# Kernel tuning notes

Hardware: AMD Instinct MI355X
Metric: run time of the kernel (lower is better)

Reference implementation:

```python
import jax, jax.numpy as jnp
import numpy as np

C_IN, C_OUT, K = 64, 64, 3
KK = K * K


def _conv3x3(x, w, b):
    # x: [B, Cin, H, W], w: [Cout, Cin, 3, 3], b: [Cout] or None. stride 1, pad 1.
    y = jax.lax.conv_general_dilated(
        x, w, window_strides=(1, 1), padding=((1, 1), (1, 1)),
        dimension_numbers=("NCHW", "OIHW", "NCHW"))
    if b is not None:
        y = y + b[None, :, None, None]
    return y


def _deform_conv2d(x, offset, mask, weight):
    # torchvision.ops.deform_conv2d with stride=1, pad=1, dilation=1, 1 offset group.
    # x: [B,C,H,W]; offset: [B,2*KK,H,W] (per-tap (dy,dx)); mask: [B,KK,H,W];
    # weight: [O,C,K,K]
    B, C, H, W = x.shape
    O = weight.shape[0]
    ky, kx = jnp.meshgrid(jnp.arange(K), jnp.arange(K), indexing="ij")
    hs = jnp.arange(H)
    ws = jnp.arange(W)
    # base sample positions per tap k=(ky*K+kx): [KK,H,W]
    base_y = (hs[:, None] - 1)[None] + ky.reshape(KK, 1, 1)
    base_x = (ws[None, :] - 1)[None] + kx.reshape(KK, 1, 1)
    off = offset.reshape(B, KK, 2, H, W)
    py = base_y[None].astype(x.dtype) + off[:, :, 0]  # [B,KK,H,W]
    px = base_x[None].astype(x.dtype) + off[:, :, 1]

    y0 = jnp.floor(py)
    x0 = jnp.floor(px)
    wy = py - y0  # bilinear fractional weights
    wx = px - x0
    y0i = y0.astype(jnp.int32)
    x0i = x0.astype(jnp.int32)

    imflat = x.reshape(B, C, H * W)

    def gather_b(im, idx):  # im: [C,HW], idx: [KK,H,W] -> [C,KK,H,W]
        return im[:, idx]

    val = jnp.zeros((B, C, KK, H, W), x.dtype)
    for dy, dx in ((0, 0), (0, 1), (1, 0), (1, 1)):
        yc = y0i + dy
        xc = x0i + dx
        valid = ((yc >= 0) & (yc < H) & (xc >= 0) & (xc < W)).astype(x.dtype)
        cw = (wy if dy else (1.0 - wy)) * (wx if dx else (1.0 - wx)) * valid
        idx = jnp.clip(yc, 0, H - 1) * W + jnp.clip(xc, 0, W - 1)
        g = jax.vmap(gather_b)(imflat, idx)  # [B,C,KK,H,W]
        val = val + cw[:, None] * g
    val = val * mask[:, None]  # modulation
    # contract 9-tap patches with conv weight
    return jnp.einsum("bckhw,ock->bohw", val, weight.reshape(O, C, KK))


def setup_inputs() -> dict:
    key = jax.random.key(0)
    ks = jax.random.split(key, 8)
    B, H, W = 4, 96, 96
    cin2 = 2 * C_IN + 2
    frame_i = jax.random.normal(ks[0], (B, C_IN, H, W), jnp.float32)
    frame_j = jax.random.normal(ks[1], (B, C_IN, H, W), jnp.float32)
    flow_ij = jax.random.normal(ks[2], (B, 2, H, W), jnp.float32)
    # small random weights so offsets are nonzero (zero-init would degenerate)
    w_off = jax.random.normal(ks[3], (2 * KK, cin2, K, K), jnp.float32) * 0.01
    b_off = jax.random.normal(ks[4], (2 * KK,), jnp.float32) * 0.1
    w_mod = jax.random.normal(ks[5], (KK, cin2, K, K), jnp.float32) * 0.01
    b_mod = jax.random.normal(ks[6], (KK,), jnp.float32) * 0.1
    w_reg = jax.random.normal(ks[7], (C_OUT, C_IN, K, K), jnp.float32) * (1.0 / np.sqrt(C_IN * KK))
    return {"frame_i": frame_i, "frame_j": frame_j, "flow_ij": flow_ij,
            "w_off": w_off, "b_off": b_off, "w_mod": w_mod, "b_mod": b_mod,
            "w_reg": w_reg}


def reference(frame_i, frame_j, flow_ij, w_off, b_off, w_mod, b_mod, w_reg):
    offset_input = jnp.concatenate([frame_i, frame_j, flow_ij], axis=1)
    offset = _conv3x3(offset_input, w_off, b_off)            # [B,2*KK,H,W]
    modulator = 2.0 * jax.nn.sigmoid(_conv3x3(offset_input, w_mod, b_mod))  # [B,KK,H,W]
    return _deform_conv2d(frame_j, offset, modulator, w_reg)
```

## Files before the change

### kernel.cpp

```cpp
#include <hip/hip_runtime.h>
#include <math.h>

#define BB   4
#define HH   96
#define WW   96
#define HW   (HH * WW)
#define CIN  64
#define COUT 64
#define C2B  192
#define NROW (BB * HW)
#define ZROW NROW
#define NSTRIP (NROW / 16)
#define BPX3 (NSTRIP / 8)
#define NA   (9 * 5 * 2 * 512)
#define NW   (9 * 2 * 4 * 512)
#define PXB2 (NROW / 32)
#define PWBLK 324
#define TSX  35
#define PR   55

typedef short v8s __attribute__((ext_vector_type(8)));
typedef float v4f __attribute__((ext_vector_type(4)));

__device__ __forceinline__ unsigned short f2bf(float f) {
    unsigned u = __float_as_uint(f);
    return (unsigned short)((u + 0x7FFFu + ((u >> 16) & 1u)) >> 16);
}
__device__ __forceinline__ unsigned pack2(float a, float b) {
    return (unsigned)f2bf(a) | ((unsigned)f2bf(b) << 16);
}
__device__ __forceinline__ unsigned bil2(unsigned a, unsigned b, unsigned c,
                                         unsigned d, float w00, float w01,
                                         float w10, float w11) {
    float lo = w00 * __uint_as_float(a << 16) + w01 * __uint_as_float(b << 16)
             + w10 * __uint_as_float(c << 16) + w11 * __uint_as_float(d << 16);
    float hi = w00 * __uint_as_float(a & 0xffff0000u)
             + w01 * __uint_as_float(b & 0xffff0000u)
             + w10 * __uint_as_float(c & 0xffff0000u)
             + w11 * __uint_as_float(d & 0xffff0000u);
    return pack2(lo, hi);
}

__global__ __launch_bounds__(256) void prep_kernel(
    const float* __restrict__ fi, const float* __restrict__ fj,
    const float* __restrict__ fl, const float* __restrict__ w_off,
    const float* __restrict__ w_mod, const float* __restrict__ w_reg,
    unsigned short* __restrict__ xt, unsigned short* __restrict__ wa2f,
    unsigned short* __restrict__ wb2f)
{
    int blk = blockIdx.x;
    if (blk < PXB2) {
        __shared__ __align__(16) unsigned tile[64 * TSX];
        int tid = threadIdx.x;
        int p = tid & 63, cg = tid >> 6;
        int u = blk >> 1, half = blk & 1;
        int r0 = u * 64;
        int b = r0 / HW;
        int hw = r0 - b * HW + p;
        uint4* dst = (uint4*)(xt + (size_t)r0 * C2B);
        if (half == 0) {
            const float* pi = fi + (size_t)b * CIN * HW + hw;
#pragma unroll
            for (int d = 0; d < 8; ++d) {
                int c = cg * 16 + 2 * d;
                tile[p * TSX + cg * 8 + d] =
                    pack2(pi[(size_t)c * HW], pi[(size_t)(c + 1) * HW]);
            }
            __syncthreads();
#pragma unroll
            for (int i = 0; i < 2; ++i) {
                int gq = i * 256 + tid;
                int rl = gq >> 3, c4 = gq & 7;
                const unsigned* s = &tile[rl * TSX + c4 * 4];
                uint4 v = {s[0], s[1], s[2], s[3]};
                dst[rl * 24 + c4] = v;
            }
        } else {
            const float* pj = fj + (size_t)b * CIN * HW + hw;
#pragma unroll
            for (int d = 0; d < 8; ++d) {
                int c = cg * 16 + 2 * d;
                tile[p * TSX + cg * 8 + d] =
                    pack2(pj[(size_t)c * HW], pj[(size_t)(c + 1) * HW]);
            }
            if (cg == 0) {
                const float* pf = fl + (size_t)b * 2 * HW + hw;
                tile[p * TSX + 32] = pack2(pf[0], pf[HW]);
            }
            __syncthreads();
#pragma unroll
            for (int i = 0; i < 4; ++i) {
                int gq = i * 256 + tid;
                int rl = gq >> 4, c4 = gq & 15;
                uint4 v = {0u, 0u, 0u, 0u};
                if (c4 < 8) {
                    const unsigned* s = &tile[rl * TSX + c4 * 4];
                    v.x = s[0]; v.y = s[1]; v.z = s[2]; v.w = s[3];
                } else if (c4 == 8) {
                    v.x = tile[rl * TSX + 32];
                }
                int pc4 = (c4 < 8) ? ((c4 & 3) * 2 + (c4 >> 2)) : c4;
                dst[rl * 24 + 8 + pc4] = v;
            }
        }
    } else if (blk < PXB2 + PWBLK) {
        int e = (blk - PXB2) * 256 + threadIdx.x;
        if (e < NA) {
            int t  = e / 5120;
            int r1 = e - t * 5120;
            int ks = r1 >> 10;
            int r2 = r1 & 1023;
            int nt = r2 >> 9;
            int l9 = r2 & 511;
            int l  = l9 >> 3, ee = l9 & 7;
            int m  = l & 15, g = l >> 4;
            int oc = nt * 16 + m;
            int ch = ks * 32 + g * 8 + ee;
            float v = 0.0f;
            if (oc < 27 && ch < 130) {
                if (oc < 18) v = w_off[((size_t)oc * 130 + ch) * 9 + t];
                else         v = w_mod[((size_t)(oc - 18) * 130 + ch) * 9 + t];
            }
            wa2f[e] = f2bf(v);
        } else {
            int e2 = e - NA;
            if (e2 < NW) {
                int k  = e2 >> 12;
                int r1 = e2 & 4095;
                int ks = r1 >> 11;
                int r2 = r1 & 2047;
                int nt = r2 >> 9;
                int l9 = r2 & 511;
                int l  = l9 >> 3, ee = l9 & 7;
                int m  = l & 15, g = l >> 4;
                int o  = nt * 16 + m;
                int c  = ks * 32 + g * 8 + ee;
                wb2f[e2] = f2bf(w_reg[((size_t)o * 64 + c) * 9 + k]);
            }
        }
    } else {
        if (threadIdx.x < 24) {
            uint4 z = {0u, 0u, 0u, 0u};
            ((uint4*)(xt + (size_t)ZROW * C2B))[threadIdx.x] = z;
        }
    }
}

__global__ __launch_bounds__(256, 5) void fused_kernel(
    const unsigned short* __restrict__ xt,
    const unsigned short* __restrict__ wa2f,
    const unsigned short* __restrict__ wb2f,
    const float* __restrict__ b_off, const float* __restrict__ b_mod,
    float* __restrict__ out)
{
    __shared__ __align__(16) unsigned char pool[18176];
    __shared__ float red1[4][8][64];

    uint4* patch4 = (uint4*)pool;
    float* red2   = (float*)pool;
    float* lraw   = (float*)(pool + 16384);

    int l = threadIdx.x & 63;
    int wid = __builtin_amdgcn_readfirstlane(threadIdx.x >> 6);
    int m = l & 15, g = l >> 4;
    int strip = (blockIdx.x & 7) * BPX3 + (blockIdx.x >> 3);
    int b = strip / (HW / 16);
    int hw0 = (strip - b * (HW / 16)) * 16;
    int hw = hw0 + m;
    int x = hw % WW, y = hw / WW;
    int y0b = hw0 / WW, x0b = hw0 - y0b * WW;
    int t0 = wid * 2;

#pragma unroll
    for (int i = 0; i < 5; ++i) {
        int item = i * 256 + threadIdx.x;
        if (item < 1080) {
            int run = item / 360;
            int rem = item - run * 360;
            int r18 = rem / 20;
            int c8  = rem - r18 * 20;
            int yy = y0b + run - 1;
            int xx = x0b - 1 + r18;
            bool ok = ((unsigned)yy < HH) && ((unsigned)xx < WW);
            uint4 v = {0u, 0u, 0u, 0u};
            if (ok)
                v = ((const uint4*)(xt + (size_t)(b * HW + yy * WW + xx) * C2B))[c8];
            patch4[c8 * PR + run * 18 + r18] = v;
        }
    }
    __syncthreads();

    v4f acc0 = {0.f, 0.f, 0.f, 0.f};
    v4f acc1 = {0.f, 0.f, 0.f, 0.f};
    {
        int ntap = (wid == 3) ? 3 : 2;
#pragma unroll
        for (int ti = 0; ti < 3; ++ti) {
            if (ti < ntap) {
                int t = t0 + ti;
                int r = (t / 3) * 18 + (t % 3) + m;
#pragma unroll
                for (int ks = 0; ks < 5; ++ks) {
                    int c8 = (ks == 0) ? g : (ks == 1) ? 4 + g
                           : (ks == 2) ? 8 + 2 * g : (ks == 3) ? 9 + 2 * g
                           : 16 + g;
                    v8s a = *(const v8s*)&patch4[c8 * PR + r];
                    const unsigned short* wp =
                        wa2f + ((size_t)((t * 5 + ks) * 2)) * 512 + l * 8;
                    v8s b0 = *(const v8s*)(wp);
                    v8s b1 = *(const v8s*)(wp + 512);
                    acc0 = __builtin_amdgcn_mfma_f32_16x16x32_bf16(a, b0, acc0, 0, 0, 0);
                    acc1 = __builtin_amdgcn_mfma_f32_16x16x32_bf16(a, b1, acc1, 0, 0, 0);
                }
            }
        }
    }

    {
#pragma unroll
        for (int j = 0; j < 4; ++j) red1[wid][j][l] = acc0[j];
#pragma unroll
        for (int j = 0; j < 4; ++j) red1[wid][4 + j][l] = acc1[j];
    }
    __syncthreads();

    {
#pragma unroll
        for (int jj = 0; jj < 2; ++jj) {
            int j = t0 + jj;
            float v = red1[0][j][l] + red1[1][j][l]
                    + red1[2][j][l] + red1[3][j][l];
            int r = j & 3;
            int oc = (j < 4) ? m : 16 + m;
            int pos = g * 4 + r;
            if (oc < 18) {
                lraw[pos * 28 + oc] = v + b_off[oc];
            } else if (oc < 27) {
                lraw[pos * 28 + oc] =
                    2.0f / (1.0f + __expf(-(v + b_mod[oc - 18])));
            }
        }
    }
    __syncthreads();

    v4f acc[4];
#pragma unroll
    for (int nt = 0; nt < 4; ++nt) acc[nt] = (v4f){0.f, 0.f, 0.f, 0.f};

    const unsigned short* rowb =
        xt + (size_t)(b * HW) * C2B + 64 + g * 16;

    auto do_tap = [&](int k) {
        int ky = k / 3, kx = k - 3 * ky;
        float dy = lraw[m * 28 + 2 * k];
        float dx = lraw[m * 28 + 2 * k + 1];
        float mm = lraw[m * 28 + 18 + k];

        float py = (float)(y - 1 + ky) + dy;
        float px = (float)(x - 1 + kx) + dx;
        float fy = floorf(py), fx = floorf(px);
        int   y0 = (int)fy,    x0 = (int)fx;
        float wy = py - fy,    wx = px - fx;
        int   y1 = y0 + 1,     x1 = x0 + 1;

        bool y0v = (y0 >= 0) && (y0 < HH);
        bool y1v = (y1 >= 0) && (y1 < HH);
        bool x0v = (x0 >= 0) && (x0 < WW);
        bool x1v = (x1 >= 0) && (x1 < WW);

        float w00 = (1.f - wy) * (1.f - wx) * ((y0v && x0v) ? mm : 0.f);
        float w01 = (1.f - wy) * wx         * ((y0v && x1v) ? mm : 0.f);
        float w10 = wy * (1.f - wx)         * ((y1v && x0v) ? mm : 0.f);
        float w11 = wy * wx                 * ((y1v && x1v) ? mm : 0.f);

        int y0c = min(max(y0, 0), HH - 1), y1c = min(max(y1, 0), HH - 1);
        int x0c = min(max(x0, 0), WW - 1), x1c = min(max(x1, 0), WW - 1);
        const unsigned short* r00 = rowb + (size_t)(y0c * WW + x0c) * C2B;
        const unsigned short* r01 = rowb + (size_t)(y0c * WW + x1c) * C2B;
        const unsigned short* r10 = rowb + (size_t)(y1c * WW + x0c) * C2B;
        const unsigned short* r11 = rowb + (size_t)(y1c * WW + x1c) * C2B;

        uint4 a00 = *(const uint4*)(r00);
        uint4 a01 = *(const uint4*)(r01);
        uint4 a10 = *(const uint4*)(r10);
        uint4 a11 = *(const uint4*)(r11);
        uint4 c00 = *(const uint4*)(r00 + 8);
        uint4 c01 = *(const uint4*)(r01 + 8);
        uint4 c10 = *(const uint4*)(r10 + 8);
        uint4 c11 = *(const uint4*)(r11 + 8);

        uint4 ov0, ov1;
        ov0.x = bil2(a00.x, a01.x, a10.x, a11.x, w00, w01, w10, w11);
        ov0.y = bil2(a00.y, a01.y, a10.y, a11.y, w00, w01, w10, w11);
        ov0.z = bil2(a00.z, a01.z, a10.z, a11.z, w00, w01, w10, w11);
        ov0.w = bil2(a00.w, a01.w, a10.w, a11.w, w00, w01, w10, w11);
        ov1.x = bil2(c00.x, c01.x, c10.x, c11.x, w00, w01, w10, w11);
        ov1.y = bil2(c00.y, c01.y, c10.y, c11.y, w00, w01, w10, w11);
        ov1.z = bil2(c00.z, c01.z, c10.z, c11.z, w00, w01, w10, w11);
        ov1.w = bil2(c00.w, c01.w, c10.w, c11.w, w00, w01, w10, w11);
        v8s af0 = __builtin_bit_cast(v8s, ov0);
        v8s af1 = __builtin_bit_cast(v8s, ov1);

#pragma unroll
        for (int nt = 0; nt < 4; ++nt) {
            const unsigned short* wp0 =
                wb2f + ((size_t)((k * 2 + 0) * 4 + nt)) * 512 + l * 8;
            const unsigned short* wp1 =
                wb2f + ((size_t)((k * 2 + 1) * 4 + nt)) * 512 + l * 8;
            v8s bb0 = *(const v8s*)wp0;
            v8s bb1 = *(const v8s*)wp1;
            acc[nt] = __builtin_amdgcn_mfma_f32_16x16x32_bf16(af0, bb0, acc[nt], 0, 0, 0);
            acc[nt] = __builtin_amdgcn_mfma_f32_16x16x32_bf16(af1, bb1, acc[nt], 0, 0, 0);
        }
    };

    do_tap(t0);
    do_tap(t0 + 1);
    if (wid == 3) do_tap(8);

    {
#pragma unroll
        for (int nt = 0; nt < 4; ++nt)
#pragma unroll
            for (int r = 0; r < 4; ++r)
                red2[(wid * 16 + nt * 4 + r) * 64 + l] = acc[nt][r];
    }
    __syncthreads();
    {
        v4f s = {0.f, 0.f, 0.f, 0.f};
#pragma unroll
        for (int r = 0; r < 4; ++r) {
            float t = 0.f;
#pragma unroll
            for (int sw = 0; sw < 4; ++sw)
                t += red2[(sw * 16 + wid * 4 + r) * 64 + l];
            s[r] = t;
        }
        float* op = out + ((size_t)(b * COUT + wid * 16 + m)) * HW + hw0 + g * 4;
        *(v4f*)op = s;
    }
}

extern "C" void kernel_launch(void* const* d_in, const int* in_sizes, int n_in,
                              void* d_out, int out_size, void* d_ws, size_t ws_size,
                              hipStream_t stream)
{
    const float* frame_i = (const float*)d_in[0];
    const float* frame_j = (const float*)d_in[1];
    const float* flow_ij = (const float*)d_in[2];
    const float* w_off   = (const float*)d_in[3];
    const float* b_off   = (const float*)d_in[4];
    const float* w_mod   = (const float*)d_in[5];
    const float* b_mod   = (const float*)d_in[6];
    const float* w_reg   = (const float*)d_in[7];
    float* out = (float*)d_out;

    unsigned short* xt   = (unsigned short*)d_ws;
    unsigned short* wa2f = xt + (size_t)(NROW + 1) * C2B;
    unsigned short* wb2f = wa2f + NA;

    prep_kernel<<<PXB2 + PWBLK + 1, 256, 0, stream>>>(
        frame_i, frame_j, flow_ij, w_off, w_mod, w_reg, xt, wa2f, wb2f);

    fused_kernel<<<NSTRIP, 256, 0, stream>>>(
        xt, wa2f, wb2f, b_off, b_mod, out);
}
```

Measured before the change: 123.8 us.

## Split fused kernel work across eight waves per block instead of four

Doubles the block to 512 threads and spreads the offset-conv MFMA steps (45 tap×k-slice units) and the deformable taps across eight waves. Each wave now does roughly one tap instead of two. The cross-wave reductions in LDS become eight-way, and the output is written as float2 per wave. This shortens each wave's serial MFMA chain and raises latency hiding per strip, at the cost of a larger LDS footprint (about 50KB per block), more reduction traffic and a lower blocks-per-CU bound.

```diff
diff --git a/kernel.cpp b/kernel.cpp
--- a/kernel.cpp
+++ b/kernel.cpp
@@ -146,19 +146,19 @@
     }
 }
 
-__global__ __launch_bounds__(256, 5) void fused_kernel(
+__global__ __launch_bounds__(512, 4) void fused_kernel(
     const unsigned short* __restrict__ xt,
     const unsigned short* __restrict__ wa2f,
     const unsigned short* __restrict__ wb2f,
     const float* __restrict__ b_off, const float* __restrict__ b_mod,
     float* __restrict__ out)
 {
-    __shared__ __align__(16) unsigned char pool[18176];
-    __shared__ float red1[4][8][64];
+    __shared__ __align__(16) unsigned char pool[32768];
+    __shared__ __align__(16) float red1[8][8][64];
+    __shared__ float lraw[16 * 28];
 
     uint4* patch4 = (uint4*)pool;
     float* red2   = (float*)pool;
-    float* lraw   = (float*)(pool + 16384);
 
     int l = threadIdx.x & 63;
     int wid = __builtin_amdgcn_readfirstlane(threadIdx.x >> 6);
@@ -169,11 +169,10 @@
     int hw = hw0 + m;
     int x = hw % WW, y = hw / WW;
     int y0b = hw0 / WW, x0b = hw0 - y0b * WW;
-    int t0 = wid * 2;
-
-#pragma unroll
-    for (int i = 0; i < 5; ++i) {
-        int item = i * 256 + threadIdx.x;
+
+#pragma unroll
+    for (int i = 0; i < 3; ++i) {
+        int item = i * 512 + threadIdx.x;
         if (item < 1080) {
             int run = item / 360;
             int rem = item - run * 360;
@@ -193,25 +192,23 @@
     v4f acc0 = {0.f, 0.f, 0.f, 0.f};
     v4f acc1 = {0.f, 0.f, 0.f, 0.f};
     {
-        int ntap = (wid == 3) ? 3 : 2;
-#pragma unroll
-        for (int ti = 0; ti < 3; ++ti) {
-            if (ti < ntap) {
-                int t = t0 + ti;
+        int nu = (wid < 5) ? 6 : 5;
+#pragma unroll
+        for (int i = 0; i < 6; ++i) {
+            if (i < nu) {
+                int u = wid + 8 * i;
+                int t = u / 5, ks = u - 5 * t;
                 int r = (t / 3) * 18 + (t % 3) + m;
-#pragma unroll
-                for (int ks = 0; ks < 5; ++ks) {
-                    int c8 = (ks == 0) ? g : (ks == 1) ? 4 + g
-                           : (ks == 2) ? 8 + 2 * g : (ks == 3) ? 9 + 2 * g
-                           : 16 + g;
-                    v8s a = *(const v8s*)&patch4[c8 * PR + r];
-                    const unsigned short* wp =
-                        wa2f + ((size_t)((t * 5 + ks) * 2)) * 512 + l * 8;
-                    v8s b0 = *(const v8s*)(wp);
-                    v8s b1 = *(const v8s*)(wp + 512);
-                    acc0 = __builtin_amdgcn_mfma_f32_16x16x32_bf16(a, b0, acc0, 0, 0, 0);
-                    acc1 = __builtin_amdgcn_mfma_f32_16x16x32_bf16(a, b1, acc1, 0, 0, 0);
-                }
+                int c8 = (ks == 0) ? g : (ks == 1) ? 4 + g
+                       : (ks == 2) ? 8 + 2 * g : (ks == 3) ? 9 + 2 * g
+                       : 16 + g;
+                v8s a = *(const v8s*)&patch4[c8 * PR + r];
+                const unsigned short* wp =
+                    wa2f + ((size_t)(u * 2)) * 512 + l * 8;
+                v8s b0 = *(const v8s*)(wp);
+                v8s b1 = *(const v8s*)(wp + 512);
+                acc0 = __builtin_amdgcn_mfma_f32_16x16x32_bf16(a, b0, acc0, 0, 0, 0);
+                acc1 = __builtin_amdgcn_mfma_f32_16x16x32_bf16(a, b1, acc1, 0, 0, 0);
             }
         }
     }
@@ -225,20 +222,18 @@
     __syncthreads();
 
     {
-#pragma unroll
-        for (int jj = 0; jj < 2; ++jj) {
-            int j = t0 + jj;
-            float v = red1[0][j][l] + red1[1][j][l]
-                    + red1[2][j][l] + red1[3][j][l];
-            int r = j & 3;
-            int oc = (j < 4) ? m : 16 + m;
-            int pos = g * 4 + r;
-            if (oc < 18) {
-                lraw[pos * 28 + oc] = v + b_off[oc];
-            } else if (oc < 27) {
-                lraw[pos * 28 + oc] =
-                    2.0f / (1.0f + __expf(-(v + b_mod[oc - 18])));
-            }
+        int j = wid;
+        float v = 0.f;
+#pragma unroll
+        for (int sw = 0; sw < 8; ++sw) v += red1[sw][j][l];
+        int r = j & 3;
+        int oc = (j < 4) ? m : 16 + m;
+        int pos = g * 4 + r;
+        if (oc < 18) {
+            lraw[pos * 28 + oc] = v + b_off[oc];
+        } else if (oc < 27) {
+            lraw[pos * 28 + oc] =
+                2.0f / (1.0f + __expf(-(v + b_mod[oc - 18])));
         }
     }
     __syncthreads();
@@ -314,30 +309,29 @@
         }
     };
 
-    do_tap(t0);
-    do_tap(t0 + 1);
-    if (wid == 3) do_tap(8);
+    do_tap(wid);
+    if (wid == 7) do_tap(8);
 
     {
 #pragma unroll
         for (int nt = 0; nt < 4; ++nt)
 #pragma unroll
             for (int r = 0; r < 4; ++r)
-                red2[(wid * 16 + nt * 4 + r) * 64 + l] = acc[nt][r];
+                red2[((size_t)wid * 16 + nt * 4 + r) * 64 + l] = acc[nt][r];
     }
     __syncthreads();
     {
-        v4f s = {0.f, 0.f, 0.f, 0.f};
-#pragma unroll
-        for (int r = 0; r < 4; ++r) {
-            float t = 0.f;
-#pragma unroll
-            for (int sw = 0; sw < 4; ++sw)
-                t += red2[(sw * 16 + wid * 4 + r) * 64 + l];
-            s[r] = t;
-        }
-        float* op = out + ((size_t)(b * COUT + wid * 16 + m)) * HW + hw0 + g * 4;
-        *(v4f*)op = s;
+        int nt = wid >> 1, r0 = (wid & 1) * 2;
+        float v0 = 0.f, v1 = 0.f;
+#pragma unroll
+        for (int sw = 0; sw < 8; ++sw) {
+            v0 += red2[((size_t)sw * 16 + nt * 4 + r0) * 64 + l];
+            v1 += red2[((size_t)sw * 16 + nt * 4 + r0 + 1) * 64 + l];
+        }
+        float* op = out + ((size_t)(b * COUT + nt * 16 + m)) * HW
+                  + hw0 + g * 4 + r0;
+        float2 s2 = {v0, v1};
+        *(float2*)op = s2;
     }
 }
 
@@ -362,6 +356,6 @@
     prep_kernel<<<PXB2 + PWBLK + 1, 256, 0, stream>>>(
         frame_i, frame_j, flow_ij, w_off, w_mod, w_reg, xt, wa2f, wb2f);
 
-    fused_kernel<<<NSTRIP, 256, 0, stream>>>(
+    fused_kernel<<<NSTRIP, 512, 0, stream>>>(
         xt, wa2f, wb2f, b_off, b_mod, out);
 }
```

Result: no change. 123.4 us (-0.3%).
